# Kernel tuning notes

Measured on AMD Instinct MI355X. Metric: run time of the kernel, lower is better.

Reference implementation:

```python
import jax, jax.numpy as jnp
import numpy as np

NORM_EPS = 1e-5
NUM_HEAD = 16
DIM_HEAD = 32
DIM_HIDDEN = 512
DIM_POS = 2
N, S = 4, 8192


def setup_inputs() -> dict:
    key = jax.random.key(0)
    ks = jax.random.split(key, 16)
    d = DIM_HIDDEN
    inp = {
        "Q": jax.random.normal(ks[0], (N, S, d), jnp.float32),
        "K": jax.random.normal(ks[1], (N, S, d), jnp.float32),
        "V": jax.random.normal(ks[2], (N, S, d), jnp.float32),
        "position": jax.random.uniform(ks[3], (N, S, DIM_POS), jnp.float32),
        "W_Q": jax.random.normal(ks[4], (d, d), jnp.float32) * (1.0 / np.sqrt(d)),
        "W_K": jax.random.normal(ks[5], (d, d), jnp.float32) * (1.0 / np.sqrt(d)),
        "W_V": jax.random.normal(ks[6], (d, d), jnp.float32) * (1.0 / np.sqrt(d)),
        "b_Q": jnp.zeros((d,), jnp.float32),
        "b_K": jnp.zeros((d,), jnp.float32),
        "b_V": jnp.zeros((d,), jnp.float32),
        "ln_w_K": jnp.ones((NUM_HEAD, DIM_HEAD), jnp.float32),
        "ln_b_K": jnp.zeros((NUM_HEAD, DIM_HEAD), jnp.float32),
        "ln_w_V": jnp.ones((NUM_HEAD, DIM_HEAD), jnp.float32),
        "ln_b_V": jnp.zeros((NUM_HEAD, DIM_HEAD), jnp.float32),
        # torch Linear(dim_hidden + dim_position*num_head, dim_hidden): weight [out, in]
        "fc_W": jax.random.normal(ks[7], (d, d + DIM_POS * NUM_HEAD), jnp.float32) * (1.0 / np.sqrt(d + DIM_POS * NUM_HEAD)),
        "fc_b": jnp.zeros((d,), jnp.float32),
    }
    return inp


def _proj_heads(x, W, b):
    # [N,S,D] @ [D,D] + [D] -> [N,H,S,Dh]
    n, s, d = x.shape
    y = x @ W + b
    return y.reshape(n, s, NUM_HEAD, DIM_HEAD).transpose(0, 2, 1, 3)


def _ln(x, w, b):
    # per-head layernorm over last dim; w,b: [H,Dh] broadcast as [1,H,1,Dh]
    mu = jnp.mean(x, axis=-1, keepdims=True)
    var = jnp.mean((x - mu) ** 2, axis=-1, keepdims=True)
    xn = (x - mu) * jax.lax.rsqrt(var + NORM_EPS)
    return xn * w[None, :, None, :] + b[None, :, None, :]


def reference(Q, K, V, position, W_Q, W_K, W_V, b_Q, b_K, b_V,
              ln_w_K, ln_b_K, ln_w_V, ln_b_V, fc_W, fc_b):
    n, s, d = Q.shape
    q = _proj_heads(Q, W_Q, b_Q)                    # [N,H,S,Dh]
    k = _ln(_proj_heads(K, W_K, b_K), ln_w_K, ln_b_K)
    v = _ln(_proj_heads(V, W_V, b_V), ln_w_V, ln_b_V)
    pos = jnp.broadcast_to(position[:, None, :, :], (n, NUM_HEAD, s, DIM_POS))
    q = jnp.concatenate([pos, q], axis=-1)          # [N,H,S,P+Dh]
    k = jnp.concatenate([pos, k], axis=-1)
    v = jnp.concatenate([pos, v], axis=-1)
    # Galerkin linear attention: Q @ (K^T V / seqlen), no softmax
    ktv = jnp.einsum('nhsd,nhse->nhde', k, v) / s   # [N,H,P+Dh,P+Dh]
    x = jnp.einsum('nhsd,nhde->nhse', q, ktv)       # [N,H,S,P+Dh]
    x = x.transpose(0, 2, 1, 3).reshape(n, s, NUM_HEAD * (DIM_POS + DIM_HEAD))
    return x @ fc_W.T + fc_b
```

## Files before the change

### kernel.cpp

```cpp
#include <hip/hip_runtime.h>
#include <hip/hip_bf16.h>

typedef short short8 __attribute__((ext_vector_type(8)));
typedef float f32x4 __attribute__((ext_vector_type(4)));
typedef unsigned int uint4v __attribute__((ext_vector_type(4)));

__device__ __forceinline__ short f2bf(float f) {
  unsigned u = __builtin_bit_cast(unsigned, f);
  u += 0x7fffu + ((u >> 16) & 1u);
  return (short)(u >> 16);
}
__device__ __forceinline__ float bf2f(short s) {
  unsigned u = ((unsigned)(unsigned short)s) << 16;
  return __builtin_bit_cast(float, u);
}
__device__ __forceinline__ unsigned pk2(float a, float b) {
  __hip_bfloat162 h = __float22bfloat162_rn(float2{a, b});
  unsigned u;
  __builtin_memcpy(&u, &h, 4);
  return u;
}
__device__ __forceinline__ void gl_lds16(const void* g, void* l) {
  __builtin_amdgcn_global_load_lds(
      (const __attribute__((address_space(1))) unsigned int*)g,
      (__attribute__((address_space(3))) unsigned int*)l, 16, 0, 0);
}

__global__ __launch_bounds__(256) void xc_kernel(
    const float* __restrict__ Q, const float* __restrict__ K,
    const float* __restrict__ V, short* __restrict__ Xb)
{
  const int z = blockIdx.y;
  const float* X = (z == 0) ? Q : (z == 1) ? K : V;
  short* o = Xb + (size_t)z * 32768 * 512;
  const int stride = gridDim.x * 256;
  const int total = 32768 * 512 / 8;
  for (int i = blockIdx.x * 256 + threadIdx.x; i < total; i += stride) {
    const f32x4* p = (const f32x4*)(X + (size_t)i * 8);
    f32x4 a = p[0], b = p[1];
    uint4v s;
    s[0] = pk2(a[0], a[1]); s[1] = pk2(a[2], a[3]);
    s[2] = pk2(b[0], b[1]); s[3] = pk2(b[2], b[3]);
    *(uint4v*)(o + (size_t)i * 8) = s;
  }
}

__global__ __launch_bounds__(256) void wt_kernel(
    const float* __restrict__ WQ, const float* __restrict__ WK,
    const float* __restrict__ WV, short* __restrict__ Wt)
{
  const int z = blockIdx.z;
  const float* W = (z == 0) ? WQ : (z == 1) ? WK : WV;
  short* o = Wt + (size_t)z * 512 * 512;
  __shared__ short t[64][65];
  const int k0 = blockIdx.y * 64, n0 = blockIdx.x * 64;
  const int c = threadIdx.x & 63, rb = threadIdx.x >> 6;
#pragma unroll
  for (int p = 0; p < 16; ++p) {
    const int kk = p * 4 + rb;
    t[kk][c] = f2bf(W[(size_t)(k0 + kk) * 512 + n0 + c]);
  }
  __syncthreads();
#pragma unroll
  for (int p = 0; p < 16; ++p) {
    const int nn = p * 4 + rb;
    o[(size_t)(n0 + nn) * 512 + k0 + c] = t[c][nn];
  }
}

__global__ __launch_bounds__(256) void proj_kernel(
    const short* __restrict__ Xb, const short* __restrict__ Wt,
    const float* __restrict__ bK, const float* __restrict__ bV,
    short* __restrict__ qp, short* __restrict__ kp, short* __restrict__ vp)
{
  const int phys = blockIdx.x;
  const int log_ = (phys & 7) * 384 + (phys >> 3);
  const int z = log_ >> 10;
  const int rem = log_ & 1023;
  const int row0 = (rem >> 2) * 128;
  const int col0 = (rem & 3) * 128;

  const short* X  = Xb + (size_t)z * 32768 * 512;
  const short* Wz = Wt + (size_t)z * 512 * 512;
  short* dst = (z == 0) ? qp : (z == 1) ? kp : vp;

  __shared__ short a_lds[2][128 * 32];
  __shared__ short b_lds[2][128 * 32];

  const int tid = threadIdx.x;
  const int lane = tid & 63, wv = tid >> 6;
  const int wr = wv >> 1, wc = wv & 1;
  const int fr = lane & 15, fg = lane >> 4;

  const int srow = wv * 16 + (lane >> 2);
  const int sswz = ((lane & 3) ^ (srow & 3)) * 8;
  const int sdst = (wv * 16) * 32 + lane * 8;

  f32x4 acc[4][4];
#pragma unroll
  for (int i = 0; i < 4; ++i)
#pragma unroll
    for (int j = 0; j < 4; ++j) acc[i][j] = (f32x4){0.f, 0.f, 0.f, 0.f};

#pragma unroll
  for (int i = 0; i < 2; ++i) {
    gl_lds16(X + (size_t)(row0 + i * 64 + srow) * 512 + sswz,
             &a_lds[0][(i * 64) * 32 + sdst]);
    gl_lds16(Wz + (size_t)(col0 + i * 64 + srow) * 512 + sswz,
             &b_lds[0][(i * 64) * 32 + sdst]);
  }
  __syncthreads();

  for (int t = 0; t < 16; ++t) {
    if (t < 15) {
      const int k1 = (t + 1) * 32;
      short* an = a_lds[(t + 1) & 1];
      short* bn = b_lds[(t + 1) & 1];
#pragma unroll
      for (int i = 0; i < 2; ++i) {
        gl_lds16(X + (size_t)(row0 + i * 64 + srow) * 512 + k1 + sswz,
                 &an[(i * 64) * 32 + sdst]);
        gl_lds16(Wz + (size_t)(col0 + i * 64 + srow) * 512 + k1 + sswz,
                 &bn[(i * 64) * 32 + sdst]);
      }
    }
    const short* ac = a_lds[t & 1];
    const short* bc = b_lds[t & 1];
    const int soff = (fg ^ (fr & 3)) * 8;
    short8 af[4], bfv[4];
#pragma unroll
    for (int mi = 0; mi < 4; ++mi)
      af[mi] = *(const short8*)&ac[(wr * 64 + mi * 16 + fr) * 32 + soff];
#pragma unroll
    for (int ni = 0; ni < 4; ++ni)
      bfv[ni] = *(const short8*)&bc[(wc * 64 + ni * 16 + fr) * 32 + soff];
#pragma unroll
    for (int mi = 0; mi < 4; ++mi)
#pragma unroll
      for (int ni = 0; ni < 4; ++ni)
        acc[mi][ni] = __builtin_amdgcn_mfma_f32_16x16x32_bf16(af[mi], bfv[ni], acc[mi][ni], 0, 0, 0);
    __syncthreads();
  }

#pragma unroll
  for (int ni = 0; ni < 4; ++ni) {
    const int gc = col0 + wc * 64 + ni * 16 + fr;
    const float bv = (z == 0) ? 0.0f : (z == 1) ? bK[gc] : bV[gc];
#pragma unroll
    for (int mi = 0; mi < 4; ++mi) {
#pragma unroll
      for (int r = 0; r < 4; ++r) {
        const int gr = row0 + wr * 64 + mi * 16 + fg * 4 + r;
        dst[(size_t)gr * 512 + gc] = f2bf(acc[mi][ni][r] + bv);
      }
    }
  }
}

#define SC 256
#define TP 264

__global__ __launch_bounds__(256) void ktv_kernel(
    const short* __restrict__ kp, const short* __restrict__ vp,
    const float* __restrict__ pos,
    const float* __restrict__ lnwK, const float* __restrict__ lnbK,
    const float* __restrict__ lnwV, const float* __restrict__ lnbV,
    float* __restrict__ ktv)
{
  const int nh = blockIdx.y;
  const int n = nh >> 4, h = nh & 15;
  const int s0 = blockIdx.x * SC;
  const int tid = threadIdx.x;

  __shared__ short klds[48 * TP];
  __shared__ short vlds[48 * TP];
  __shared__ float lw[2][32], lb[2][32];

  if (tid < 32) {
    lw[0][tid] = lnwK[h * 32 + tid]; lb[0][tid] = lnbK[h * 32 + tid];
    lw[1][tid] = lnwV[h * 32 + tid]; lb[1][tid] = lnbV[h * 32 + tid];
  }
  __syncthreads();

  const size_t rowix = (size_t)n * 8192 + (s0 + tid);
  {
    const short8* src = (const short8*)(kp + rowix * 512 + h * 32);
    short8 r0 = src[0], r1 = src[1], r2 = src[2], r3 = src[3];
    float x[32];
#pragma unroll
    for (int i = 0; i < 8; ++i) { x[i] = bf2f(r0[i]); x[8+i] = bf2f(r1[i]); x[16+i] = bf2f(r2[i]); x[24+i] = bf2f(r3[i]); }
    float mu = 0.f;
#pragma unroll
    for (int i = 0; i < 32; ++i) mu += x[i];
    mu *= (1.f / 32.f);
    float var = 0.f;
#pragma unroll
    for (int i = 0; i < 32; ++i) { float d = x[i] - mu; var += d * d; }
    var *= (1.f / 32.f);
    const float rstd = rsqrtf(var + 1e-5f);
#pragma unroll
    for (int d = 0; d < 32; ++d)
      klds[d * TP + tid] = f2bf((x[d] - mu) * rstd * lw[0][d] + lb[0][d]);
  }
  {
    const short8* src = (const short8*)(vp + rowix * 512 + h * 32);
    short8 r0 = src[0], r1 = src[1], r2 = src[2], r3 = src[3];
    float x[32];
#pragma unroll
    for (int i = 0; i < 8; ++i) { x[i] = bf2f(r0[i]); x[8+i] = bf2f(r1[i]); x[16+i] = bf2f(r2[i]); x[24+i] = bf2f(r3[i]); }
    float mu = 0.f;
#pragma unroll
    for (int i = 0; i < 32; ++i) mu += x[i];
    mu *= (1.f / 32.f);
    float var = 0.f;
#pragma unroll
    for (int i = 0; i < 32; ++i) { float d = x[i] - mu; var += d * d; }
    var *= (1.f / 32.f);
    const float rstd = rsqrtf(var + 1e-5f);
#pragma unroll
    for (int d = 0; d < 32; ++d)
      vlds[d * TP + tid] = f2bf((x[d] - mu) * rstd * lw[1][d] + lb[1][d]);
  }
  {
    const short p0 = f2bf(pos[rowix * 2]);
    const short p1 = f2bf(pos[rowix * 2 + 1]);
    klds[32 * TP + tid] = p0; klds[33 * TP + tid] = p1;
    vlds[32 * TP + tid] = p0; vlds[33 * TP + tid] = p1;
  }
  __syncthreads();

  const int wv = tid >> 6, lane = tid & 63;
  if (wv < 3) {
    const int fr = lane & 15, fg = lane >> 4;
    f32x4 acc[3];
#pragma unroll
    for (int i = 0; i < 3; ++i) acc[i] = (f32x4){0.f, 0.f, 0.f, 0.f};
    for (int kk = 0; kk < SC; kk += 32) {
      short8 a = *(const short8*)&klds[(wv * 16 + fr) * TP + kk + fg * 8];
#pragma unroll
      for (int ni = 0; ni < 3; ++ni) {
        short8 b = *(const short8*)&vlds[(ni * 16 + fr) * TP + kk + fg * 8];
        acc[ni] = __builtin_amdgcn_mfma_f32_16x16x32_bf16(a, b, acc[ni], 0, 0, 0);
      }
    }
#pragma unroll
    for (int ni = 0; ni < 3; ++ni) {
      const int ei = ni * 16 + fr;
      if (ei < 34) {
        const int er = (ei < 32) ? ei + 2 : ei - 32;
#pragma unroll
        for (int r = 0; r < 4; ++r) {
          const int di = wv * 16 + fg * 4 + r;
          if (di < 34) {
            const int dr = (di < 32) ? di + 2 : di - 32;
            atomicAdd(&ktv[((size_t)nh * 34 + dr) * 34 + er], acc[ni][r]);
          }
        }
      }
    }
  }
}

__global__ __launch_bounds__(256) void sbuild_kernel(
    const float* __restrict__ ktv, const float* __restrict__ fcW,
    const float* __restrict__ bQ, short* __restrict__ St, float* __restrict__ Pp3)
{
  const int nh = blockIdx.x;
  const int n = nh >> 4, h = nh & 15;
  const int jq = blockIdx.y;
  __shared__ float g[34 * 34];
  __shared__ float bq8[8];
  for (int i = threadIdx.x; i < 34 * 34; i += 256)
    g[i] = ktv[(size_t)nh * 34 * 34 + i] * (1.f / 8192.f);
  if (threadIdx.x < 8) bq8[threadIdx.x] = bQ[h * 32 + jq * 8 + threadIdx.x];
  __syncthreads();

  for (int o = threadIdx.x; o < 512; o += 256) {
    float wcol[34];
#pragma unroll
    for (int e = 0; e < 34; ++e) wcol[e] = fcW[(size_t)o * 544 + h * 34 + e];
    float rv = 0.f;
    short* srow = St + ((size_t)n * 512 + o) * 512 + h * 32 + jq * 8;
#pragma unroll
    for (int jj = 0; jj < 8; ++jj) {
      const int j = jq * 8 + jj;
      float s = 0.f;
#pragma unroll
      for (int e = 0; e < 34; ++e) s += g[(j + 2) * 34 + e] * wcol[e];
      srow[jj] = f2bf(s);
      rv += bq8[jj] * s;
    }
    atomicAdd(&Pp3[((size_t)n * 3 + 2) * 512 + o], rv);
    if (jq == 0) {
      float p0 = 0.f, p1 = 0.f;
#pragma unroll
      for (int e = 0; e < 34; ++e) { p0 += g[e] * wcol[e]; p1 += g[34 + e] * wcol[e]; }
      atomicAdd(&Pp3[((size_t)n * 3 + 0) * 512 + o], p0);
      atomicAdd(&Pp3[((size_t)n * 3 + 1) * 512 + o], p1);
    }
  }
}

__global__ __launch_bounds__(256) void fuse_kernel(
    const short* __restrict__ qp, const short* __restrict__ St,
    const float* __restrict__ pos, const float* __restrict__ Pp3,
    const float* __restrict__ fcb, float* __restrict__ out)
{
  const int phys = blockIdx.x;
  const int log_ = (phys & 7) * 128 + (phys >> 3);
  const int n = log_ >> 8;
  const int rem = log_ & 255;
  const int row0 = (rem >> 2) * 128;
  const int col0 = (rem & 3) * 128;

  const short* A = qp + (size_t)n * 8192 * 512;
  const short* B = St + (size_t)n * 512 * 512;

  __shared__ short a_lds[2][128 * 32];
  __shared__ short b_lds[2][128 * 32];

  const int tid = threadIdx.x;
  const int lane = tid & 63, wv = tid >> 6;
  const int wr = wv >> 1, wc = wv & 1;
  const int fr = lane & 15, fg = lane >> 4;

  const int srow = wv * 16 + (lane >> 2);
  const int sswz = ((lane & 3) ^ (srow & 3)) * 8;
  const int sdst = (wv * 16) * 32 + lane * 8;

  f32x4 acc[4][4];
#pragma unroll
  for (int i = 0; i < 4; ++i)
#pragma unroll
    for (int j = 0; j < 4; ++j) acc[i][j] = (f32x4){0.f, 0.f, 0.f, 0.f};

#pragma unroll
  for (int i = 0; i < 2; ++i) {
    gl_lds16(A + (size_t)(row0 + i * 64 + srow) * 512 + sswz,
             &a_lds[0][(i * 64) * 32 + sdst]);
    gl_lds16(B + (size_t)(col0 + i * 64 + srow) * 512 + sswz,
             &b_lds[0][(i * 64) * 32 + sdst]);
  }
  __syncthreads();

  for (int t = 0; t < 16; ++t) {
    if (t < 15) {
      const int k1 = (t + 1) * 32;
      short* an = a_lds[(t + 1) & 1];
      short* bn = b_lds[(t + 1) & 1];
#pragma unroll
      for (int i = 0; i < 2; ++i) {
        gl_lds16(A + (size_t)(row0 + i * 64 + srow) * 512 + k1 + sswz,
                 &an[(i * 64) * 32 + sdst]);
        gl_lds16(B + (size_t)(col0 + i * 64 + srow) * 512 + k1 + sswz,
                 &bn[(i * 64) * 32 + sdst]);
      }
    }
    const short* ac = a_lds[t & 1];
    const short* bc = b_lds[t & 1];
    const int soff = (fg ^ (fr & 3)) * 8;
    short8 af[4], bfv[4];
#pragma unroll
    for (int mi = 0; mi < 4; ++mi)
      af[mi] = *(const short8*)&ac[(wr * 64 + mi * 16 + fr) * 32 + soff];
#pragma unroll
    for (int ni = 0; ni < 4; ++ni)
      bfv[ni] = *(const short8*)&bc[(wc * 64 + ni * 16 + fr) * 32 + soff];
#pragma unroll
    for (int mi = 0; mi < 4; ++mi)
#pragma unroll
      for (int ni = 0; ni < 4; ++ni)
        acc[mi][ni] = __builtin_amdgcn_mfma_f32_16x16x32_bf16(af[mi], bfv[ni], acc[mi][ni], 0, 0, 0);
    __syncthreads();
  }

  float pp0[4], pp1[4], rv[4];
#pragma unroll
  for (int ni = 0; ni < 4; ++ni) {
    const int gc = col0 + wc * 64 + ni * 16 + fr;
    pp0[ni] = Pp3[((size_t)n * 3 + 0) * 512 + gc];
    pp1[ni] = Pp3[((size_t)n * 3 + 1) * 512 + gc];
    rv[ni]  = Pp3[((size_t)n * 3 + 2) * 512 + gc] + fcb[gc];
  }
#pragma unroll
  for (int mi = 0; mi < 4; ++mi) {
#pragma unroll
    for (int r = 0; r < 4; ++r) {
      const int gr = row0 + wr * 64 + mi * 16 + fg * 4 + r;
      const float* pr = pos + ((size_t)n * 8192 + gr) * 2;
      const float q0 = pr[0], q1 = pr[1];
#pragma unroll
      for (int ni = 0; ni < 4; ++ni) {
        const int gc = col0 + wc * 64 + ni * 16 + fr;
        out[((size_t)n * 8192 + gr) * 512 + gc] =
            acc[mi][ni][r] + pp0[ni] * q0 + pp1[ni] * q1 + rv[ni];
      }
    }
  }
}

extern "C" void kernel_launch(void* const* d_in, const int* in_sizes, int n_in,
                              void* d_out, int out_size, void* d_ws, size_t ws_size,
                              hipStream_t stream) {
  const float* Q    = (const float*)d_in[0];
  const float* Kin  = (const float*)d_in[1];
  const float* Vin  = (const float*)d_in[2];
  const float* pos  = (const float*)d_in[3];
  const float* WQ   = (const float*)d_in[4];
  const float* WK   = (const float*)d_in[5];
  const float* WV   = (const float*)d_in[6];
  const float* bQ   = (const float*)d_in[7];
  const float* bK   = (const float*)d_in[8];
  const float* bV   = (const float*)d_in[9];
  const float* lnwK = (const float*)d_in[10];
  const float* lnbK = (const float*)d_in[11];
  const float* lnwV = (const float*)d_in[12];
  const float* lnbV = (const float*)d_in[13];
  const float* fcW  = (const float*)d_in[14];
  const float* fcb  = (const float*)d_in[15];

  char* ws = (char*)d_ws;
  const size_t XB_B  = (size_t)3 * 32768 * 512 * 2;
  const size_t P_B   = (size_t)32768 * 512 * 2;
  const size_t KTV_B = (size_t)64 * 34 * 34 * 4;
  const size_t ST_B  = (size_t)4 * 512 * 512 * 2;
  const size_t WT_B  = (size_t)3 * 512 * 512 * 2;
  const size_t PP_B  = (size_t)4 * 3 * 512 * 4;
  short* Xb  = (short*)ws;
  short* qp  = (short*)(ws + XB_B);
  short* kp  = (short*)(ws + XB_B + P_B);
  short* vp  = (short*)(ws + XB_B + 2 * P_B);
  float* ktv = (float*)(ws + XB_B + 3 * P_B);
  short* St  = (short*)(ws + XB_B + 3 * P_B + KTV_B);
  short* Wt  = (short*)(ws + XB_B + 3 * P_B + KTV_B + ST_B);
  float* Pp3 = (float*)(ws + XB_B + 3 * P_B + KTV_B + ST_B + WT_B);

  (void)hipMemsetAsync(ktv, 0, KTV_B, stream);
  (void)hipMemsetAsync(Pp3, 0, PP_B, stream);
  hipLaunchKernelGGL(xc_kernel, dim3(1024, 3), dim3(256), 0, stream, Q, Kin, Vin, Xb);
  hipLaunchKernelGGL(wt_kernel, dim3(8, 8, 3), dim3(256), 0, stream, WQ, WK, WV, Wt);
  hipLaunchKernelGGL(proj_kernel, dim3(3072), dim3(256), 0, stream,
                     Xb, Wt, bK, bV, qp, kp, vp);
  hipLaunchKernelGGL(ktv_kernel, dim3(32, 64), dim3(256), 0, stream,
                     kp, vp, pos, lnwK, lnbK, lnwV, lnbV, ktv);
  hipLaunchKernelGGL(sbuild_kernel, dim3(64, 4), dim3(256), 0, stream,
                     ktv, fcW, bQ, St, Pp3);
  hipLaunchKernelGGL(fuse_kernel, dim3(1024), dim3(256), 0, stream,
                     qp, St, pos, Pp3, fcb, (float*)d_out);
}
```

Baseline: 236.2 us.

## Fold W_Q into per-batch output matrix and read fp32 inputs directly in GEMMs

```diff
diff --git a/kernel.cpp b/kernel.cpp
--- a/kernel.cpp
+++ b/kernel.cpp
@@ -25,32 +25,19 @@
       (const __attribute__((address_space(1))) unsigned int*)g,
       (__attribute__((address_space(3))) unsigned int*)l, 16, 0, 0);
 }
-
-__global__ __launch_bounds__(256) void xc_kernel(
-    const float* __restrict__ Q, const float* __restrict__ K,
-    const float* __restrict__ V, short* __restrict__ Xb)
-{
-  const int z = blockIdx.y;
-  const float* X = (z == 0) ? Q : (z == 1) ? K : V;
-  short* o = Xb + (size_t)z * 32768 * 512;
-  const int stride = gridDim.x * 256;
-  const int total = 32768 * 512 / 8;
-  for (int i = blockIdx.x * 256 + threadIdx.x; i < total; i += stride) {
-    const f32x4* p = (const f32x4*)(X + (size_t)i * 8);
-    f32x4 a = p[0], b = p[1];
-    uint4v s;
-    s[0] = pk2(a[0], a[1]); s[1] = pk2(a[2], a[3]);
-    s[2] = pk2(b[0], b[1]); s[3] = pk2(b[2], b[3]);
-    *(uint4v*)(o + (size_t)i * 8) = s;
-  }
+__device__ __forceinline__ short8 cvt8(f32x4 a, f32x4 b) {
+  uint4v u;
+  u[0] = pk2(a[0], a[1]); u[1] = pk2(a[2], a[3]);
+  u[2] = pk2(b[0], b[1]); u[3] = pk2(b[2], b[3]);
+  return __builtin_bit_cast(short8, u);
 }
 
 __global__ __launch_bounds__(256) void wt_kernel(
-    const float* __restrict__ WQ, const float* __restrict__ WK,
-    const float* __restrict__ WV, short* __restrict__ Wt)
+    const float* __restrict__ WK, const float* __restrict__ WV,
+    short* __restrict__ Wt)
 {
   const int z = blockIdx.z;
-  const float* W = (z == 0) ? WQ : (z == 1) ? WK : WV;
+  const float* W = (z == 0) ? WK : WV;
   short* o = Wt + (size_t)z * 512 * 512;
   __shared__ short t[64][65];
   const int k0 = blockIdx.y * 64, n0 = blockIdx.x * 64;
@@ -69,22 +56,23 @@
 }
 
 __global__ __launch_bounds__(256) void proj_kernel(
-    const short* __restrict__ Xb, const short* __restrict__ Wt,
+    const float* __restrict__ Kin, const float* __restrict__ Vin,
+    const short* __restrict__ Wt,
     const float* __restrict__ bK, const float* __restrict__ bV,
-    short* __restrict__ qp, short* __restrict__ kp, short* __restrict__ vp)
+    short* __restrict__ kp, short* __restrict__ vp)
 {
   const int phys = blockIdx.x;
-  const int log_ = (phys & 7) * 384 + (phys >> 3);
+  const int log_ = (phys & 7) * 256 + (phys >> 3);
   const int z = log_ >> 10;
   const int rem = log_ & 1023;
   const int row0 = (rem >> 2) * 128;
   const int col0 = (rem & 3) * 128;
 
-  const short* X  = Xb + (size_t)z * 32768 * 512;
-  const short* Wz = Wt + (size_t)z * 512 * 512;
-  short* dst = (z == 0) ? qp : (z == 1) ? kp : vp;
-
-  __shared__ short a_lds[2][128 * 32];
+  const float* X    = z ? Vin : Kin;
+  const short* Bsrc = Wt + (size_t)z * 512 * 512;
+  const float* bias = z ? bV : bK;
+  short* dst        = z ? vp : kp;
+
   __shared__ short b_lds[2][128 * 32];
 
   const int tid = threadIdx.x;
@@ -95,6 +83,12 @@
   const int srow = wv * 16 + (lane >> 2);
   const int sswz = ((lane & 3) ^ (srow & 3)) * 8;
   const int sdst = (wv * 16) * 32 + lane * 8;
+  const int soff = (fg ^ (fr & 3)) * 8;
+
+  const float* arow[4];
+#pragma unroll
+  for (int mi = 0; mi < 4; ++mi)
+    arow[mi] = X + (size_t)(row0 + wr * 64 + mi * 16 + fr) * 512 + fg * 8;
 
   f32x4 acc[4][4];
 #pragma unroll
@@ -102,50 +96,54 @@
 #pragma unroll
     for (int j = 0; j < 4; ++j) acc[i][j] = (f32x4){0.f, 0.f, 0.f, 0.f};
 
-#pragma unroll
-  for (int i = 0; i < 2; ++i) {
-    gl_lds16(X + (size_t)(row0 + i * 64 + srow) * 512 + sswz,
-             &a_lds[0][(i * 64) * 32 + sdst]);
-    gl_lds16(Wz + (size_t)(col0 + i * 64 + srow) * 512 + sswz,
+  f32x4 va[4][2];
+#pragma unroll
+  for (int mi = 0; mi < 4; ++mi) {
+    va[mi][0] = *(const f32x4*)(arow[mi]);
+    va[mi][1] = *(const f32x4*)(arow[mi] + 4);
+  }
+#pragma unroll
+  for (int i = 0; i < 2; ++i)
+    gl_lds16(Bsrc + (size_t)(col0 + i * 64 + srow) * 512 + sswz,
              &b_lds[0][(i * 64) * 32 + sdst]);
-  }
   __syncthreads();
 
   for (int t = 0; t < 16; ++t) {
+    short8 af[4];
+#pragma unroll
+    for (int mi = 0; mi < 4; ++mi) af[mi] = cvt8(va[mi][0], va[mi][1]);
+    short8 bfv[4];
+    const short* bc = b_lds[t & 1];
+#pragma unroll
+    for (int ni = 0; ni < 4; ++ni)
+      bfv[ni] = *(const short8*)&bc[(wc * 64 + ni * 16 + fr) * 32 + soff];
     if (t < 15) {
       const int k1 = (t + 1) * 32;
-      short* an = a_lds[(t + 1) & 1];
       short* bn = b_lds[(t + 1) & 1];
 #pragma unroll
-      for (int i = 0; i < 2; ++i) {
-        gl_lds16(X + (size_t)(row0 + i * 64 + srow) * 512 + k1 + sswz,
-                 &an[(i * 64) * 32 + sdst]);
-        gl_lds16(Wz + (size_t)(col0 + i * 64 + srow) * 512 + k1 + sswz,
+      for (int i = 0; i < 2; ++i)
+        gl_lds16(Bsrc + (size_t)(col0 + i * 64 + srow) * 512 + k1 + sswz,
                  &bn[(i * 64) * 32 + sdst]);
-      }
-    }
-    const short* ac = a_lds[t & 1];
-    const short* bc = b_lds[t & 1];
-    const int soff = (fg ^ (fr & 3)) * 8;
-    short8 af[4], bfv[4];
-#pragma unroll
-    for (int mi = 0; mi < 4; ++mi)
-      af[mi] = *(const short8*)&ac[(wr * 64 + mi * 16 + fr) * 32 + soff];
-#pragma unroll
-    for (int ni = 0; ni < 4; ++ni)
-      bfv[ni] = *(const short8*)&bc[(wc * 64 + ni * 16 + fr) * 32 + soff];
+#pragma unroll
+      for (int mi = 0; mi < 4; ++mi) {
+        va[mi][0] = *(const f32x4*)(arow[mi] + k1);
+        va[mi][1] = *(const f32x4*)(arow[mi] + k1 + 4);
+      }
+    }
+    __builtin_amdgcn_s_setprio(1);
 #pragma unroll
     for (int mi = 0; mi < 4; ++mi)
 #pragma unroll
       for (int ni = 0; ni < 4; ++ni)
         acc[mi][ni] = __builtin_amdgcn_mfma_f32_16x16x32_bf16(af[mi], bfv[ni], acc[mi][ni], 0, 0, 0);
+    __builtin_amdgcn_s_setprio(0);
     __syncthreads();
   }
 
 #pragma unroll
   for (int ni = 0; ni < 4; ++ni) {
     const int gc = col0 + wc * 64 + ni * 16 + fr;
-    const float bv = (z == 0) ? 0.0f : (z == 1) ? bK[gc] : bV[gc];
+    const float bv = bias[gc];
 #pragma unroll
     for (int mi = 0; mi < 4; ++mi) {
 #pragma unroll
@@ -263,7 +261,7 @@
 
 __global__ __launch_bounds__(256) void sbuild_kernel(
     const float* __restrict__ ktv, const float* __restrict__ fcW,
-    const float* __restrict__ bQ, short* __restrict__ St, float* __restrict__ Pp3)
+    const float* __restrict__ bQ, float* __restrict__ St, float* __restrict__ Pp3)
 {
   const int nh = blockIdx.x;
   const int n = nh >> 4, h = nh & 15;
@@ -280,14 +278,14 @@
 #pragma unroll
     for (int e = 0; e < 34; ++e) wcol[e] = fcW[(size_t)o * 544 + h * 34 + e];
     float rv = 0.f;
-    short* srow = St + ((size_t)n * 512 + o) * 512 + h * 32 + jq * 8;
+    float* srow = St + ((size_t)n * 512 + o) * 512 + h * 32 + jq * 8;
 #pragma unroll
     for (int jj = 0; jj < 8; ++jj) {
       const int j = jq * 8 + jj;
       float s = 0.f;
 #pragma unroll
       for (int e = 0; e < 34; ++e) s += g[(j + 2) * 34 + e] * wcol[e];
-      srow[jj] = f2bf(s);
+      srow[jj] = s;
       rv += bq8[jj] * s;
     }
     atomicAdd(&Pp3[((size_t)n * 3 + 2) * 512 + o], rv);
@@ -301,8 +299,83 @@
   }
 }
 
+__global__ __launch_bounds__(256) void cbuild_kernel(
+    const float* __restrict__ St, const float* __restrict__ WQ,
+    short* __restrict__ Ct)
+{
+  const int n = blockIdx.z;
+  const int row0 = blockIdx.y * 128;
+  const int col0 = blockIdx.x * 128;
+  const float* A = St + (size_t)n * 512 * 512;
+  const float* B = WQ;
+
+  __shared__ short a_lds[128 * 32];
+  __shared__ short b_lds2[128 * 32];
+
+  const int tid = threadIdx.x;
+  const int lane = tid & 63, wv = tid >> 6;
+  const int wr = wv >> 1, wc = wv & 1;
+  const int fr = lane & 15, fg = lane >> 4;
+  const int ar = tid >> 1, ak = (tid & 1) * 16;
+
+  f32x4 acc[4][4];
+#pragma unroll
+  for (int i = 0; i < 4; ++i)
+#pragma unroll
+    for (int j = 0; j < 4; ++j) acc[i][j] = (f32x4){0.f, 0.f, 0.f, 0.f};
+
+  for (int k0 = 0; k0 < 512; k0 += 32) {
+    __syncthreads();
+    {
+      const f32x4* ap = (const f32x4*)(A + (size_t)(row0 + ar) * 512 + k0 + ak);
+      f32x4 f0 = ap[0], f1 = ap[1], f2 = ap[2], f3 = ap[3];
+      uint4v s0, s1;
+      s0[0] = pk2(f0[0], f0[1]); s0[1] = pk2(f0[2], f0[3]);
+      s0[2] = pk2(f1[0], f1[1]); s0[3] = pk2(f1[2], f1[3]);
+      s1[0] = pk2(f2[0], f2[1]); s1[1] = pk2(f2[2], f2[3]);
+      s1[2] = pk2(f3[0], f3[1]); s1[3] = pk2(f3[2], f3[3]);
+      *(uint4v*)&a_lds[ar * 32 + ak] = s0;
+      *(uint4v*)&a_lds[ar * 32 + ak + 8] = s1;
+      const f32x4* bp = (const f32x4*)(B + (size_t)(col0 + ar) * 512 + k0 + ak);
+      f32x4 g0 = bp[0], g1 = bp[1], g2 = bp[2], g3 = bp[3];
+      s0[0] = pk2(g0[0], g0[1]); s0[1] = pk2(g0[2], g0[3]);
+      s0[2] = pk2(g1[0], g1[1]); s0[3] = pk2(g1[2], g1[3]);
+      s1[0] = pk2(g2[0], g2[1]); s1[1] = pk2(g2[2], g2[3]);
+      s1[2] = pk2(g3[0], g3[1]); s1[3] = pk2(g3[2], g3[3]);
+      *(uint4v*)&b_lds2[ar * 32 + ak] = s0;
+      *(uint4v*)&b_lds2[ar * 32 + ak + 8] = s1;
+    }
+    __syncthreads();
+
+    short8 af[4], bfr[4];
+#pragma unroll
+    for (int mi = 0; mi < 4; ++mi)
+      af[mi] = *(const short8*)&a_lds[(wr * 64 + mi * 16 + fr) * 32 + fg * 8];
+#pragma unroll
+    for (int ni = 0; ni < 4; ++ni)
+      bfr[ni] = *(const short8*)&b_lds2[(wc * 64 + ni * 16 + fr) * 32 + fg * 8];
+#pragma unroll
+    for (int mi = 0; mi < 4; ++mi)
+#pragma unroll
+      for (int ni = 0; ni < 4; ++ni)
+        acc[mi][ni] = __builtin_amdgcn_mfma_f32_16x16x32_bf16(af[mi], bfr[ni], acc[mi][ni], 0, 0, 0);
+  }
+
+#pragma unroll
+  for (int ni = 0; ni < 4; ++ni) {
+    const int gc = col0 + wc * 64 + ni * 16 + fr;
+#pragma unroll
+    for (int mi = 0; mi < 4; ++mi)
+#pragma unroll
+      for (int r = 0; r < 4; ++r) {
+        const int gr = row0 + wr * 64 + mi * 16 + fg * 4 + r;
+        Ct[((size_t)n * 512 + gr) * 512 + gc] = f2bf(acc[mi][ni][r]);
+      }
+  }
+}
+
 __global__ __launch_bounds__(256) void fuse_kernel(
-    const short* __restrict__ qp, const short* __restrict__ St,
+    const float* __restrict__ Q, const short* __restrict__ Ct,
     const float* __restrict__ pos, const float* __restrict__ Pp3,
     const float* __restrict__ fcb, float* __restrict__ out)
 {
@@ -313,10 +386,11 @@
   const int row0 = (rem >> 2) * 128;
   const int col0 = (rem & 3) * 128;
 
-  const short* A = qp + (size_t)n * 8192 * 512;
-  const short* B = St + (size_t)n * 512 * 512;
-
-  __shared__ short a_lds[2][128 * 32];
+  const float* X    = Q + (size_t)n * 8192 * 512;
+  const short* Bsrc = Ct + (size_t)n * 512 * 512;
+  float* dstf       = out + (size_t)n * 8192 * 512;
+  const float* posn = pos + (size_t)n * 8192 * 2;
+
   __shared__ short b_lds[2][128 * 32];
 
   const int tid = threadIdx.x;
@@ -327,6 +401,12 @@
   const int srow = wv * 16 + (lane >> 2);
   const int sswz = ((lane & 3) ^ (srow & 3)) * 8;
   const int sdst = (wv * 16) * 32 + lane * 8;
+  const int soff = (fg ^ (fr & 3)) * 8;
+
+  const float* arow[4];
+#pragma unroll
+  for (int mi = 0; mi < 4; ++mi)
+    arow[mi] = X + (size_t)(row0 + wr * 64 + mi * 16 + fr) * 512 + fg * 8;
 
   f32x4 acc[4][4];
 #pragma unroll
@@ -334,43 +414,47 @@
 #pragma unroll
     for (int j = 0; j < 4; ++j) acc[i][j] = (f32x4){0.f, 0.f, 0.f, 0.f};
 
-#pragma unroll
-  for (int i = 0; i < 2; ++i) {
-    gl_lds16(A + (size_t)(row0 + i * 64 + srow) * 512 + sswz,
-             &a_lds[0][(i * 64) * 32 + sdst]);
-    gl_lds16(B + (size_t)(col0 + i * 64 + srow) * 512 + sswz,
+  f32x4 va[4][2];
+#pragma unroll
+  for (int mi = 0; mi < 4; ++mi) {
+    va[mi][0] = *(const f32x4*)(arow[mi]);
+    va[mi][1] = *(const f32x4*)(arow[mi] + 4);
+  }
+#pragma unroll
+  for (int i = 0; i < 2; ++i)
+    gl_lds16(Bsrc + (size_t)(col0 + i * 64 + srow) * 512 + sswz,
              &b_lds[0][(i * 64) * 32 + sdst]);
-  }
   __syncthreads();
 
   for (int t = 0; t < 16; ++t) {
+    short8 af[4];
+#pragma unroll
+    for (int mi = 0; mi < 4; ++mi) af[mi] = cvt8(va[mi][0], va[mi][1]);
+    short8 bfv[4];
+    const short* bc = b_lds[t & 1];
+#pragma unroll
+    for (int ni = 0; ni < 4; ++ni)
+      bfv[ni] = *(const short8*)&bc[(wc * 64 + ni * 16 + fr) * 32 + soff];
     if (t < 15) {
       const int k1 = (t + 1) * 32;
-      short* an = a_lds[(t + 1) & 1];
       short* bn = b_lds[(t + 1) & 1];
 #pragma unroll
-      for (int i = 0; i < 2; ++i) {
-        gl_lds16(A + (size_t)(row0 + i * 64 + srow) * 512 + k1 + sswz,
-                 &an[(i * 64) * 32 + sdst]);
-        gl_lds16(B + (size_t)(col0 + i * 64 + srow) * 512 + k1 + sswz,
+      for (int i = 0; i < 2; ++i)
+        gl_lds16(Bsrc + (size_t)(col0 + i * 64 + srow) * 512 + k1 + sswz,
                  &bn[(i * 64) * 32 + sdst]);
-      }
-    }
-    const short* ac = a_lds[t & 1];
-    const short* bc = b_lds[t & 1];
-    const int soff = (fg ^ (fr & 3)) * 8;
-    short8 af[4], bfv[4];
-#pragma unroll
-    for (int mi = 0; mi < 4; ++mi)
-      af[mi] = *(const short8*)&ac[(wr * 64 + mi * 16 + fr) * 32 + soff];
-#pragma unroll
-    for (int ni = 0; ni < 4; ++ni)
-      bfv[ni] = *(const short8*)&bc[(wc * 64 + ni * 16 + fr) * 32 + soff];
+#pragma unroll
+      for (int mi = 0; mi < 4; ++mi) {
+        va[mi][0] = *(const f32x4*)(arow[mi] + k1);
+        va[mi][1] = *(const f32x4*)(arow[mi] + k1 + 4);
+      }
+    }
+    __builtin_amdgcn_s_setprio(1);
 #pragma unroll
     for (int mi = 0; mi < 4; ++mi)
 #pragma unroll
       for (int ni = 0; ni < 4; ++ni)
         acc[mi][ni] = __builtin_amdgcn_mfma_f32_16x16x32_bf16(af[mi], bfv[ni], acc[mi][ni], 0, 0, 0);
+    __builtin_amdgcn_s_setprio(0);
     __syncthreads();
   }
 
@@ -387,12 +471,12 @@
 #pragma unroll
     for (int r = 0; r < 4; ++r) {
       const int gr = row0 + wr * 64 + mi * 16 + fg * 4 + r;
-      const float* pr = pos + ((size_t)n * 8192 + gr) * 2;
-      const float q0 = pr[0], q1 = pr[1];
+      const float q0 = posn[(size_t)gr * 2];
+      const float q1 = posn[(size_t)gr * 2 + 1];
 #pragma unroll
       for (int ni = 0; ni < 4; ++ni) {
         const int gc = col0 + wc * 64 + ni * 16 + fr;
-        out[((size_t)n * 8192 + gr) * 512 + gc] =
+        dstf[(size_t)gr * 512 + gc] =
             acc[mi][ni][r] + pp0[ni] * q0 + pp1[ni] * q1 + rv[ni];
       }
     }
@@ -420,31 +504,31 @@
   const float* fcb  = (const float*)d_in[15];
 
   char* ws = (char*)d_ws;
-  const size_t XB_B  = (size_t)3 * 32768 * 512 * 2;
-  const size_t P_B   = (size_t)32768 * 512 * 2;
+  const size_t KP_B  = (size_t)4 * 8192 * 512 * 2;
   const size_t KTV_B = (size_t)64 * 34 * 34 * 4;
-  const size_t ST_B  = (size_t)4 * 512 * 512 * 2;
-  const size_t WT_B  = (size_t)3 * 512 * 512 * 2;
+  const size_t ST_B  = (size_t)4 * 512 * 512 * 4;
+  const size_t CT_B  = (size_t)4 * 512 * 512 * 2;
+  const size_t WT_B  = (size_t)2 * 512 * 512 * 2;
   const size_t PP_B  = (size_t)4 * 3 * 512 * 4;
-  short* Xb  = (short*)ws;
-  short* qp  = (short*)(ws + XB_B);
-  short* kp  = (short*)(ws + XB_B + P_B);
-  short* vp  = (short*)(ws + XB_B + 2 * P_B);
-  float* ktv = (float*)(ws + XB_B + 3 * P_B);
-  short* St  = (short*)(ws + XB_B + 3 * P_B + KTV_B);
-  short* Wt  = (short*)(ws + XB_B + 3 * P_B + KTV_B + ST_B);
-  float* Pp3 = (float*)(ws + XB_B + 3 * P_B + KTV_B + ST_B + WT_B);
+  short* kp  = (short*)ws;
+  short* vp  = (short*)(ws + KP_B);
+  float* ktv = (float*)(ws + 2 * KP_B);
+  float* St  = (float*)(ws + 2 * KP_B + KTV_B);
+  short* Ct  = (short*)(ws + 2 * KP_B + KTV_B + ST_B);
+  short* Wt  = (short*)(ws + 2 * KP_B + KTV_B + ST_B + CT_B);
+  float* Pp3 = (float*)(ws + 2 * KP_B + KTV_B + ST_B + CT_B + WT_B);
 
   (void)hipMemsetAsync(ktv, 0, KTV_B, stream);
   (void)hipMemsetAsync(Pp3, 0, PP_B, stream);
-  hipLaunchKernelGGL(xc_kernel, dim3(1024, 3), dim3(256), 0, stream, Q, Kin, Vin, Xb);
-  hipLaunchKernelGGL(wt_kernel, dim3(8, 8, 3), dim3(256), 0, stream, WQ, WK, WV, Wt);
-  hipLaunchKernelGGL(proj_kernel, dim3(3072), dim3(256), 0, stream,
-                     Xb, Wt, bK, bV, qp, kp, vp);
+  hipLaunchKernelGGL(wt_kernel, dim3(8, 8, 2), dim3(256), 0, stream, WK, WV, Wt);
+  hipLaunchKernelGGL(proj_kernel, dim3(2048), dim3(256), 0, stream,
+                     Kin, Vin, Wt, bK, bV, kp, vp);
   hipLaunchKernelGGL(ktv_kernel, dim3(32, 64), dim3(256), 0, stream,
                      kp, vp, pos, lnwK, lnbK, lnwV, lnbV, ktv);
   hipLaunchKernelGGL(sbuild_kernel, dim3(64, 4), dim3(256), 0, stream,
                      ktv, fcW, bQ, St, Pp3);
+  hipLaunchKernelGGL(cbuild_kernel, dim3(4, 4, 4), dim3(256), 0, stream,
+                     St, WQ, Ct);
   hipLaunchKernelGGL(fuse_kernel, dim3(1024), dim3(256), 0, stream,
-                     qp, St, pos, Pp3, fcb, (float*)d_out);
-}
+                     Q, Ct, pos, Pp3, fcb, (float*)d_out);
+}
```

New measurement: 307.8 us. +30.3%, slower.
